# Optimization experiments

Measured on AMD Instinct MI355X. Metric: run time of the kernel, lower is better.

Reference implementation:

```python
import jax, jax.numpy as jnp
import numpy as np

N_SRC = 200_000
N_DST = 40_000
N_EDGES = 8_000_000
N_LAYERS = 6
TH_R = 0.4  # dR threshold for class_name == 'supercharged'


def delta_r(phi0, eta0, phi1, eta1):
    deta = eta0 - eta1
    dphi = phi0 - phi1
    pi = jnp.float32(np.pi)
    dphi = jnp.where(dphi > pi, dphi - 2 * pi, dphi)
    dphi = jnp.where(dphi < -pi, dphi + 2 * pi, dphi)
    return jnp.sqrt(deta ** 2 + dphi ** 2)


def setup_inputs() -> dict:
    key = jax.random.key(0)
    ks = jax.random.split(key, 8)
    src = jax.random.randint(ks[0], (N_EDGES,), 0, N_SRC, dtype=jnp.int32)
    dst = jax.random.randint(ks[1], (N_EDGES,), 0, N_DST, dtype=jnp.int32)
    energy = jax.random.uniform(ks[2], (N_SRC,), dtype=jnp.float32)
    layer = jax.random.randint(ks[3], (N_SRC,), 0, N_LAYERS, dtype=jnp.int32)
    eta_src = jax.random.normal(ks[4], (N_SRC,), dtype=jnp.float32)
    phi_src = jax.random.normal(ks[5], (N_SRC,), dtype=jnp.float32)
    eta_dst = jax.random.normal(ks[6], (N_DST,), dtype=jnp.float32)
    phi_dst = jax.random.normal(ks[7], (N_DST,), dtype=jnp.float32)
    return {"src": src, "dst": dst, "energy": energy, "layer": layer,
            "eta_src": eta_src, "phi_src": phi_src,
            "eta_dst": eta_dst, "phi_dst": phi_dst}


def reference(src, dst, energy, layer, eta_src, phi_src, eta_dst, phi_dst):
    # --- edge_function_dR_reco: per-edge gather + dR mask ---
    dR = delta_r(phi_src[src], eta_src[src], phi_dst[dst], eta_dst[dst])  # [E]
    edge_dR_labels = (dR < TH_R).astype(energy.dtype)                      # [E]

    # --- particle_message: 6 layer-bucketed masked energies per edge ---
    e = energy[src] * edge_dR_labels                                       # [E]
    onehot = (layer[src][:, None] == jnp.arange(N_LAYERS)[None, :])        # [E,6]
    msgs = e[:, None] * onehot.astype(e.dtype)                             # [E,6]

    # --- particle_update: ragged mailbox sum + sample std per dst node ---
    seg_sum = jax.ops.segment_sum(msgs, dst, num_segments=N_DST)           # [N_dst,6]
    seg_sq = jax.ops.segment_sum(msgs * msgs, dst, num_segments=N_DST)     # [N_dst,6]
    deg = jax.ops.segment_sum(jnp.ones_like(e), dst, num_segments=N_DST)   # [N_dst]
    deg = deg[:, None]

    valid = deg > 1
    mean = seg_sum / jnp.maximum(deg, 1.0)
    # unbiased sample variance, as in torch.std(dim=1)
    var = (seg_sq - deg * mean * mean) / jnp.maximum(deg - 1.0, 1.0)
    var = jnp.maximum(var, 0.0)
    safe = var > 0
    std = jnp.where(safe, jnp.sqrt(jnp.where(safe, var, 1.0)), 0.0)
    std = jnp.where(valid, std, 0.0)

    return jnp.concatenate([seg_sum, std], axis=1)  # [N_dst, 12]
```

## Files before the change

### kernel.cpp

```cpp
#include <hip/hip_runtime.h>
#include <math.h>

#define N_SRC 200000
#define N_DST 40000
#define N_EDGES 8000000
#define N_LAYERS 6
#define N_OUT (N_DST * 12)

#define EBLK 512
#define ETPB 512

typedef int vint4 __attribute__((ext_vector_type(4)));

__device__ float4 g_psrc[N_SRC];
__device__ float2 g_pdst[N_DST];
__device__ unsigned int g_partial[EBLK][N_DST / 4];

__global__ __launch_bounds__(256) void pack_kernel(
        const float* __restrict__ energy, const int* __restrict__ layer,
        const float* __restrict__ eta_s, const float* __restrict__ phi_s,
        const float* __restrict__ eta_d, const float* __restrict__ phi_d,
        float* __restrict__ out) {
    int i = blockIdx.x * blockDim.x + threadIdx.x;
    if (i < N_SRC) {
        float4 p;
        p.x = energy[i];
        p.y = eta_s[i];
        p.z = phi_s[i];
        p.w = __int_as_float(layer[i]);
        g_psrc[i] = p;
    }
    if (i < N_DST) g_pdst[i] = make_float2(eta_d[i], phi_d[i]);
    if (i < N_OUT) out[i] = 0.0f;
}

__device__ __forceinline__ void edge_compute(unsigned int* __restrict__ bins,
                                             int s, int d,
                                             float* __restrict__ out) {
    atomicAdd(&bins[d >> 2], 1u << ((d & 3) * 8));

    float4 p = g_psrc[s];
    float2 q = g_pdst[d];

    const float pif   = 3.14159265358979323846f;
    const float twopi = 6.28318530717958647692f;
    float deta = p.y - q.x;
    float dphi = p.z - q.y;
    dphi = (dphi >  pif) ? dphi - twopi : dphi;
    dphi = (dphi < -pif) ? dphi + twopi : dphi;
    float dr = sqrtf(deta * deta + dphi * dphi);
    if (dr < 0.4f) {
        int   l = __float_as_int(p.w);
        float e = p.x;
        float* base = out + (size_t)d * 12;
        atomicAdd(base + l,     e);
        atomicAdd(base + 6 + l, e * e);
    }
}

__global__ __launch_bounds__(ETPB, 8) void edge_kernel(
        const vint4* __restrict__ src4, const vint4* __restrict__ dst4,
        float* __restrict__ out) {
    __shared__ unsigned int bins[N_DST / 4];

    for (int i = threadIdx.x; i < N_DST / 4; i += ETPB) bins[i] = 0u;
    __syncthreads();

    const int nvec = N_EDGES / 4;
    for (int v = blockIdx.x * ETPB + threadIdx.x; v < nvec; v += EBLK * ETPB) {
        vint4 s4 = __builtin_nontemporal_load(src4 + v);
        vint4 d4 = __builtin_nontemporal_load(dst4 + v);
        edge_compute(bins, s4.x, d4.x, out);
        edge_compute(bins, s4.y, d4.y, out);
        edge_compute(bins, s4.z, d4.z, out);
        edge_compute(bins, s4.w, d4.w, out);
    }
    __syncthreads();

    unsigned int* po = &g_partial[blockIdx.x][0];
    for (int i = threadIdx.x; i < N_DST / 4; i += ETPB)
        __builtin_nontemporal_store(bins[i], po + i);
}

__device__ __forceinline__ void finalize_one(float* __restrict__ out, int d, float dg) {
    float mean_den = fmaxf(dg, 1.0f);
    float var_den  = fmaxf(dg - 1.0f, 1.0f);
    bool  valid    = dg > 1.0f;
    float* base = out + (size_t)d * 12;
#pragma unroll
    for (int l = 0; l < N_LAYERS; ++l) {
        float s = base[l];
        float q = base[6 + l];
        float mean = s / mean_den;
        float t = dg * mean;
        t = t * mean;
        float var = (q - t) / var_den;
        var = fmaxf(var, 0.0f);
        float sd = (var > 0.0f) ? sqrtf(var) : 0.0f;
        if (!valid) sd = 0.0f;
        base[6 + l] = sd;
    }
}

__global__ __launch_bounds__(256) void finalize_kernel(float* __restrict__ out) {
    int t = blockIdx.x * blockDim.x + threadIdx.x;
    if (t >= N_DST / 4) return;
    unsigned int c0 = 0, c1 = 0, c2 = 0, c3 = 0;
#pragma unroll 8
    for (int p = 0; p < EBLK; ++p) {
        unsigned int w = g_partial[p][t];
        c0 += w & 255u;
        c1 += (w >> 8) & 255u;
        c2 += (w >> 16) & 255u;
        c3 += (w >> 24);
    }
    finalize_one(out, 4 * t + 0, (float)c0);
    finalize_one(out, 4 * t + 1, (float)c1);
    finalize_one(out, 4 * t + 2, (float)c2);
    finalize_one(out, 4 * t + 3, (float)c3);
}

extern "C" void kernel_launch(void* const* d_in, const int* in_sizes, int n_in,
                              void* d_out, int out_size, void* d_ws, size_t ws_size,
                              hipStream_t stream) {
    const int*   src     = (const int*)  d_in[0];
    const int*   dst     = (const int*)  d_in[1];
    const float* energy  = (const float*)d_in[2];
    const int*   layer   = (const int*)  d_in[3];
    const float* eta_src = (const float*)d_in[4];
    const float* phi_src = (const float*)d_in[5];
    const float* eta_dst = (const float*)d_in[6];
    const float* phi_dst = (const float*)d_in[7];
    float* out = (float*)d_out;

    pack_kernel<<<(N_OUT + 255) / 256, 256, 0, stream>>>(
        energy, layer, eta_src, phi_src, eta_dst, phi_dst, out);

    edge_kernel<<<EBLK, ETPB, 0, stream>>>(
        (const vint4*)src, (const vint4*)dst, out);

    finalize_kernel<<<(N_DST / 4 + 255) / 256, 256, 0, stream>>>(out);
}
```

Measured before the change: 233.3 us.

## Partition edge kernel by destination slices with shared-memory dst coordinates

Splits destination nodes into 8 slices. Each block loads its slice's eta/phi into shared memory and scans one edge chunk, processing only edges whose destination falls in that slice. This removes the global gather of dst coordinates and shrinks the per-block degree bins, but every edge index is read once per slice, relying on cache locality between neighbouring blocks. The finalize kernel is adapted to the new partial-count layout.

```diff
diff --git a/kernel.cpp b/kernel.cpp
--- a/kernel.cpp
+++ b/kernel.cpp
@@ -7,19 +7,22 @@
 #define N_LAYERS 6
 #define N_OUT (N_DST * 12)
 
-#define EBLK 512
+#define NSLICE 8
+#define SLICE_DST (N_DST / NSLICE)
+#define NCHUNK 128
 #define ETPB 512
+#define NEBLK (NSLICE * NCHUNK)
+#define VPC (N_EDGES / 4 / NCHUNK)
+#define BINW (SLICE_DST / 4)
 
 typedef int vint4 __attribute__((ext_vector_type(4)));
 
 __device__ float4 g_psrc[N_SRC];
-__device__ float2 g_pdst[N_DST];
-__device__ unsigned int g_partial[EBLK][N_DST / 4];
+__device__ unsigned int g_part8[NEBLK][BINW];
 
 __global__ __launch_bounds__(256) void pack_kernel(
         const float* __restrict__ energy, const int* __restrict__ layer,
         const float* __restrict__ eta_s, const float* __restrict__ phi_s,
-        const float* __restrict__ eta_d, const float* __restrict__ phi_d,
         float* __restrict__ out) {
     int i = blockIdx.x * blockDim.x + threadIdx.x;
     if (i < N_SRC) {
@@ -30,55 +33,61 @@
         p.w = __int_as_float(layer[i]);
         g_psrc[i] = p;
     }
-    if (i < N_DST) g_pdst[i] = make_float2(eta_d[i], phi_d[i]);
     if (i < N_OUT) out[i] = 0.0f;
 }
 
-__device__ __forceinline__ void edge_compute(unsigned int* __restrict__ bins,
-                                             int s, int d,
-                                             float* __restrict__ out) {
-    atomicAdd(&bins[d >> 2], 1u << ((d & 3) * 8));
+__global__ __launch_bounds__(ETPB) void edge_kernel(
+        const vint4* __restrict__ src4, const vint4* __restrict__ dst4,
+        const float* __restrict__ eta_d, const float* __restrict__ phi_d,
+        float* __restrict__ out) {
+    __shared__ float2 slice[SLICE_DST];
+    __shared__ unsigned int bins[BINW];
 
-    float4 p = g_psrc[s];
-    float2 q = g_pdst[d];
+    const int bid   = blockIdx.x;
+    const int sl    = (bid >> 3) & (NSLICE - 1);
+    const int chunk = ((bid >> 6) << 3) | (bid & 7);
+    const int dbase = sl * SLICE_DST;
+
+    for (int i = threadIdx.x; i < SLICE_DST; i += ETPB)
+        slice[i] = make_float2(eta_d[dbase + i], phi_d[dbase + i]);
+    for (int i = threadIdx.x; i < BINW; i += ETPB) bins[i] = 0u;
+    __syncthreads();
+
+    const vint4* sp = src4 + (size_t)chunk * VPC;
+    const vint4* dp = dst4 + (size_t)chunk * VPC;
 
     const float pif   = 3.14159265358979323846f;
     const float twopi = 6.28318530717958647692f;
-    float deta = p.y - q.x;
-    float dphi = p.z - q.y;
-    dphi = (dphi >  pif) ? dphi - twopi : dphi;
-    dphi = (dphi < -pif) ? dphi + twopi : dphi;
-    float dr = sqrtf(deta * deta + dphi * dphi);
-    if (dr < 0.4f) {
-        int   l = __float_as_int(p.w);
-        float e = p.x;
-        float* base = out + (size_t)d * 12;
-        atomicAdd(base + l,     e);
-        atomicAdd(base + 6 + l, e * e);
-    }
-}
 
-__global__ __launch_bounds__(ETPB, 8) void edge_kernel(
-        const vint4* __restrict__ src4, const vint4* __restrict__ dst4,
-        float* __restrict__ out) {
-    __shared__ unsigned int bins[N_DST / 4];
-
-    for (int i = threadIdx.x; i < N_DST / 4; i += ETPB) bins[i] = 0u;
-    __syncthreads();
-
-    const int nvec = N_EDGES / 4;
-    for (int v = blockIdx.x * ETPB + threadIdx.x; v < nvec; v += EBLK * ETPB) {
-        vint4 s4 = __builtin_nontemporal_load(src4 + v);
-        vint4 d4 = __builtin_nontemporal_load(dst4 + v);
-        edge_compute(bins, s4.x, d4.x, out);
-        edge_compute(bins, s4.y, d4.y, out);
-        edge_compute(bins, s4.z, d4.z, out);
-        edge_compute(bins, s4.w, d4.w, out);
+    for (int v = threadIdx.x; v < VPC; v += ETPB) {
+        vint4 s4 = sp[v];
+        vint4 d4 = dp[v];
+#pragma unroll
+        for (int j = 0; j < 4; ++j) {
+            int dl = d4[j] - dbase;
+            if ((unsigned)dl < (unsigned)SLICE_DST) {
+                atomicAdd(&bins[dl >> 2], 1u << ((dl & 3) * 8));
+                float4 p = g_psrc[s4[j]];
+                float2 q = slice[dl];
+                float deta = p.y - q.x;
+                float dphi = p.z - q.y;
+                dphi = (dphi >  pif) ? dphi - twopi : dphi;
+                dphi = (dphi < -pif) ? dphi + twopi : dphi;
+                float dr = sqrtf(deta * deta + dphi * dphi);
+                if (dr < 0.4f) {
+                    int   l = __float_as_int(p.w);
+                    float e = p.x;
+                    float* base = out + (size_t)(dbase + dl) * 12;
+                    atomicAdd(base + l,     e);
+                    atomicAdd(base + 6 + l, e * e);
+                }
+            }
+        }
     }
     __syncthreads();
 
-    unsigned int* po = &g_partial[blockIdx.x][0];
-    for (int i = threadIdx.x; i < N_DST / 4; i += ETPB)
+    unsigned int* po = &g_part8[bid][0];
+    for (int i = threadIdx.x; i < BINW; i += ETPB)
         __builtin_nontemporal_store(bins[i], po + i);
 }
 
@@ -104,20 +113,24 @@
 
 __global__ __launch_bounds__(256) void finalize_kernel(float* __restrict__ out) {
     int t = blockIdx.x * blockDim.x + threadIdx.x;
-    if (t >= N_DST / 4) return;
+    if (t >= NSLICE * BINW) return;
+    int sl = t / BINW;
+    int w  = t % BINW;
     unsigned int c0 = 0, c1 = 0, c2 = 0, c3 = 0;
 #pragma unroll 8
-    for (int p = 0; p < EBLK; ++p) {
-        unsigned int w = g_partial[p][t];
-        c0 += w & 255u;
-        c1 += (w >> 8) & 255u;
-        c2 += (w >> 16) & 255u;
-        c3 += (w >> 24);
+    for (int k = 0; k < NCHUNK; ++k) {
+        int bid = ((k >> 3) << 6) | (sl << 3) | (k & 7);
+        unsigned int word = g_part8[bid][w];
+        c0 += word & 255u;
+        c1 += (word >> 8) & 255u;
+        c2 += (word >> 16) & 255u;
+        c3 += (word >> 24);
     }
-    finalize_one(out, 4 * t + 0, (float)c0);
-    finalize_one(out, 4 * t + 1, (float)c1);
-    finalize_one(out, 4 * t + 2, (float)c2);
-    finalize_one(out, 4 * t + 3, (float)c3);
+    int d0 = sl * SLICE_DST + w * 4;
+    finalize_one(out, d0 + 0, (float)c0);
+    finalize_one(out, d0 + 1, (float)c1);
+    finalize_one(out, d0 + 2, (float)c2);
+    finalize_one(out, d0 + 3, (float)c3);
 }
 
 extern "C" void kernel_launch(void* const* d_in, const int* in_sizes, int n_in,
@@ -134,10 +147,10 @@
     float* out = (float*)d_out;
 
     pack_kernel<<<(N_OUT + 255) / 256, 256, 0, stream>>>(
-        energy, layer, eta_src, phi_src, eta_dst, phi_dst, out);
+        energy, layer, eta_src, phi_src, out);
 
-    edge_kernel<<<EBLK, ETPB, 0, stream>>>(
-        (const vint4*)src, (const vint4*)dst, out);
+    edge_kernel<<<NEBLK, ETPB, 0, stream>>>(
+        (const vint4*)src, (const vint4*)dst, eta_dst, phi_dst, out);
 
-    finalize_kernel<<<(N_DST / 4 + 255) / 256, 256, 0, stream>>>(out);
+    finalize_kernel<<<(NSLICE * BINW + 255) / 256, 256, 0, stream>>>(out);
 }
```

Measured after the change: 288.8 us. 23.7% more time.
